# Performance work log

Measured on AMD Instinct MI355X. Metric: run time of the kernel, lower is better.

Reference implementation:

```python
import jax, jax.numpy as jnp
import numpy as np

B, D, H = 131072, 8, 128


def setup_inputs() -> dict:
    key = jax.random.key(0)
    ks = jax.random.split(key, 8)
    s1 = 1.0 / np.sqrt(D + 1)
    s2 = 1.0 / np.sqrt(H)
    return {
        "z": jax.random.normal(ks[0], (B, D), dtype=jnp.float32),
        "logp_z": jnp.zeros((B, 1), dtype=jnp.float32),
        "t": jax.random.uniform(ks[1], (1,), dtype=jnp.float32),
        "W1": jax.random.normal(ks[2], (D + 1, H), dtype=jnp.float32) * s1,
        "b1": jnp.zeros((H,), dtype=jnp.float32),
        "W2": jax.random.normal(ks[3], (H, H), dtype=jnp.float32) * s2,
        "b2": jnp.zeros((H,), dtype=jnp.float32),
        "W3": jax.random.normal(ks[4], (H, D), dtype=jnp.float32) * s2,
        "b3": jnp.zeros((D,), dtype=jnp.float32),
    }


def _net_single(z_i, t_scalar, W1, b1, W2, b2, W3, b3):
    # z_i: [D] -> dz/dt: [D]; FFJORD-style MLP on concat([z, t])
    x = jnp.concatenate([z_i, t_scalar[None]])  # [D+1]
    h = jnp.tanh(x @ W1 + b1)
    h = jnp.tanh(h @ W2 + b2)
    return h @ W3 + b3


def reference(z, logp_z, t, W1, b1, W2, b2, W3, b3):
    t_scalar = t.reshape(())

    def f_i(z_i):
        return _net_single(z_i, t_scalar, W1, b1, W2, b2, W3, b3)

    # dz/dt for every sample (batched forward)
    dz_dt = jax.vmap(f_i)(z)  # [B, D]
    # Exact Jacobian trace: fused forward-mode batched Jacobian (replaces the
    # original's D sequential autograd.grad reverse-mode calls)
    jac = jax.vmap(jax.jacfwd(f_i))(z)  # [B, D, D]
    trace = jnp.einsum("bii->b", jac)  # [B]
    dlogp_z_dt = -trace[:, None]  # [B, 1]
    return (dz_dt, dlogp_z_dt)
```

## Files before the change

### kernel.cpp

```cpp
#include <hip/hip_runtime.h>
#include <hip/hip_bf16.h>

#define BATCH 131072
#define PITCH 136

typedef __bf16 bf16x8 __attribute__((ext_vector_type(8)));
typedef float floatx4 __attribute__((ext_vector_type(4)));

__device__ __forceinline__ float fast_tanh(float x) {
    float e = __expf(2.0f * x);
    return 1.0f - 2.0f * __builtin_amdgcn_rcpf(e + 1.0f);
}


__global__ void prep_kernel(const float* __restrict__ W1,
                            const float* __restrict__ W2,
                            const float* __restrict__ W3,
                            __bf16* __restrict__ ws) {
    int idx = blockIdx.x * 256 + threadIdx.x;
    if (idx < 16384) {
        int j = idx & 7, q = (idx >> 3) & 3, n = (idx >> 5) & 127, kb = idx >> 12;
        int k = kb * 32 + q * 8 + j;
        ws[idx] = (__bf16)W2[k * 128 + n];
        float c = 0.0f;
        #pragma unroll
        for (int d = 0; d < 8; ++d) c += W3[k * 8 + d] * W1[d * 128 + n];
        ws[16384 + idx] = (__bf16)(W2[n * 128 + k] * c);
    } else if (idx < 20480) {
        int t = idx - 16384;
        int j = t & 7, q = (t >> 3) & 3, n = t >> 5;
        int k = q * 8 + j;
        ws[32768 + t] = (k < 9) ? (__bf16)W1[k * 128 + n] : (__bf16)0.0f;
    } else if (idx < 22528) {
        int t = idx - 20480;
        int j = t & 7, q = (t >> 3) & 3, n = (t >> 5) & 15, kb = t >> 9;
        int k = kb * 32 + q * 8 + j;
        ws[36864 + t] = (n < 8) ? (__bf16)W3[k * 8 + n] : (__bf16)0.0f;
    }
}

__global__ __launch_bounds__(256, 2) void cnf_main(
        const float* __restrict__ z, const float* __restrict__ t_ptr,
        const float* __restrict__ b1g, const float* __restrict__ b2g,
        const float* __restrict__ b3g, const __bf16* __restrict__ ws,
        float* __restrict__ out) {
    __shared__ __bf16 sW2s[16384];
    __shared__ __bf16 sW1s[4096];
    __shared__ float sb1[128];
    __shared__ float sb2[128];
    __shared__ __bf16 tile[4][16 * PITCH];

    const int tid = threadIdx.x;
    {
        uint4* dst = (uint4*)sW2s;
        const uint4* src = (const uint4*)ws;
        for (int i = tid; i < 2048; i += 256) dst[i] = src[i];
        uint4* dst1 = (uint4*)sW1s;
        const uint4* src1 = (const uint4*)(ws + 32768);
        for (int i = tid; i < 512; i += 256) dst1[i] = src1[i];
        if (tid < 128) { sb1[tid] = b1g[tid]; sb2[tid] = b2g[tid]; }
    }
    __syncthreads();

    const int lane = tid & 63;
    const int w = tid >> 6;
    const int p = lane & 15;
    const int q = lane >> 4;
    __bf16* T = tile[w];
    const float tval = t_ptr[0];
    const float b3v = (p < 8) ? b3g[p] : 0.0f;
    const bf16x8* W2sv = (const bf16x8*)sW2s;
    const bf16x8* W1sv = (const bf16x8*)sW1s;
    const bf16x8* GTv  = (const bf16x8*)(ws + 16384);
    const bf16x8* W3v  = (const bf16x8*)(ws + 36864);

    for (int it = 0; it < 4; ++it) {
        const int s0 = blockIdx.x * 256 + it * 64 + w * 16;

        bf16x8 ax;
        #pragma unroll
        for (int j = 0; j < 8; ++j) ax[j] = (__bf16)0.0f;
        if (q == 0) {
            const float4 z0 = ((const float4*)(z + (size_t)(s0 + p) * 8))[0];
            const float4 z1 = ((const float4*)(z + (size_t)(s0 + p) * 8))[1];
            ax[0] = (__bf16)z0.x; ax[1] = (__bf16)z0.y;
            ax[2] = (__bf16)z0.z; ax[3] = (__bf16)z0.w;
            ax[4] = (__bf16)z1.x; ax[5] = (__bf16)z1.y;
            ax[6] = (__bf16)z1.z; ax[7] = (__bf16)z1.w;
        } else if (q == 1) {
            ax[0] = (__bf16)tval;
        }

        float a1c[32];
        #pragma unroll
        for (int nt = 0; nt < 8; ++nt) {
            const int n = nt * 16 + p;
            floatx4 acc = {0.f, 0.f, 0.f, 0.f};
            acc = __builtin_amdgcn_mfma_f32_16x16x32_bf16(ax, W1sv[n * 4 + q], acc, 0, 0, 0);
            const float bn = sb1[n];
            #pragma unroll
            for (int r = 0; r < 4; ++r) {
                const float h1 = fast_tanh(acc[r] + bn);
                a1c[nt * 4 + r] = __builtin_fmaf(-h1, h1, 1.0f);
                T[(q * 4 + r) * PITCH + n] = (__bf16)h1;
            }
        }
        bf16x8 ah[4];
        #pragma unroll
        for (int kb = 0; kb < 4; ++kb)
            ah[kb] = *(const bf16x8*)&T[p * PITCH + kb * 32 + q * 8];

        float h2c[32];
        #pragma unroll
        for (int nt = 0; nt < 8; ++nt) {
            const int n = nt * 16 + p;
            floatx4 acc = {0.f, 0.f, 0.f, 0.f};
            #pragma unroll
            for (int kb = 0; kb < 4; ++kb)
                acc = __builtin_amdgcn_mfma_f32_16x16x32_bf16(
                        ah[kb], W2sv[(kb * 128 + n) * 4 + q], acc, 0, 0, 0);
            const float bn = sb2[n];
            #pragma unroll
            for (int r = 0; r < 4; ++r) {
                const float h2 = fast_tanh(acc[r] + bn);
                h2c[nt * 4 + r] = h2;
                const float a2 = __builtin_fmaf(-h2, h2, 1.0f);
                T[(q * 4 + r) * PITCH + n] = (__bf16)a2;
            }
        }
        bf16x8 aa[4];
        #pragma unroll
        for (int kb = 0; kb < 4; ++kb)
            aa[kb] = *(const bf16x8*)&T[p * PITCH + kb * 32 + q * 8];

        float tr[4] = {0.f, 0.f, 0.f, 0.f};
        #pragma unroll
        for (int nt = 0; nt < 8; ++nt) {
            const int n = nt * 16 + p;
            floatx4 acc = {0.f, 0.f, 0.f, 0.f};
            #pragma unroll
            for (int kb = 0; kb < 4; ++kb)
                acc = __builtin_amdgcn_mfma_f32_16x16x32_bf16(
                        aa[kb], GTv[(kb * 128 + n) * 4 + q], acc, 0, 0, 0);
            #pragma unroll
            for (int r = 0; r < 4; ++r)
                tr[r] = __builtin_fmaf(a1c[nt * 4 + r], acc[r], tr[r]);
        }

        #pragma unroll
        for (int i = 0; i < 32; ++i)
            T[(q * 4 + (i & 3)) * PITCH + (i >> 2) * 16 + p] = (__bf16)h2c[i];
        bf16x8 ah2[4];
        #pragma unroll
        for (int kb = 0; kb < 4; ++kb)
            ah2[kb] = *(const bf16x8*)&T[p * PITCH + kb * 32 + q * 8];

        floatx4 acc3 = {0.f, 0.f, 0.f, 0.f};
        #pragma unroll
        for (int kb = 0; kb < 4; ++kb)
            acc3 = __builtin_amdgcn_mfma_f32_16x16x32_bf16(
                    ah2[kb], W3v[(kb * 16 + p) * 4 + q], acc3, 0, 0, 0);
        if (p < 8) {
            #pragma unroll
            for (int r = 0; r < 4; ++r)
                out[(size_t)(s0 + q * 4 + r) * 8 + p] = acc3[r] + b3v;
        }

        #pragma unroll
        for (int r = 0; r < 4; ++r) {
            float v = tr[r];
            v += __shfl_xor(v, 1, 64);
            v += __shfl_xor(v, 2, 64);
            v += __shfl_xor(v, 4, 64);
            v += __shfl_xor(v, 8, 64);
            tr[r] = v;
        }
        if (p == 0) {
            #pragma unroll
            for (int r = 0; r < 4; ++r)
                out[(size_t)BATCH * 8 + s0 + q * 4 + r] = -tr[r];
        }
    }
}

extern "C" void kernel_launch(void* const* d_in, const int* in_sizes, int n_in,
                              void* d_out, int out_size, void* d_ws, size_t ws_size,
                              hipStream_t stream) {
    const float* z  = (const float*)d_in[0];
    const float* t  = (const float*)d_in[2];
    const float* W1 = (const float*)d_in[3];
    const float* b1 = (const float*)d_in[4];
    const float* W2 = (const float*)d_in[5];
    const float* b2 = (const float*)d_in[6];
    const float* W3 = (const float*)d_in[7];
    const float* b3 = (const float*)d_in[8];
    __bf16* ws = (__bf16*)d_ws;
    float* out = (float*)d_out;

    prep_kernel<<<88, 256, 0, stream>>>(W1, W2, W3, ws);
    cnf_main<<<512, 256, 0, stream>>>(z, t, b1, b2, b3, ws, out);
}
```

Before: 104.8 us.

## Read weights from global memory instead of LDS and raise occupancy

Stops staging W2 and W1 in shared memory and has the MFMA operands read them straight from global memory, relying on L1/L2 caching. This shrinks LDS per block so four blocks per CU fit, and the launch bounds and grid double to match (1024 blocks, two iterations each). The layer-2 activations are kept packed as bf16 pairs to cut register pressure. The risk is more global/L2 traffic and latency on the weight loads in exchange for higher occupancy and no per-block staging cost.

```diff
diff --git a/kernel.cpp b/kernel.cpp
--- a/kernel.cpp
+++ b/kernel.cpp
@@ -10,6 +10,12 @@
 __device__ __forceinline__ float fast_tanh(float x) {
     float e = __expf(2.0f * x);
     return 1.0f - 2.0f * __builtin_amdgcn_rcpf(e + 1.0f);
+}
+
+__device__ __forceinline__ unsigned bpack(float a, float b) {
+    unsigned short ua = __builtin_bit_cast(unsigned short, (__bf16)a);
+    unsigned short ub = __builtin_bit_cast(unsigned short, (__bf16)b);
+    return (unsigned)ua | ((unsigned)ub << 16);
 }
 
 
@@ -39,27 +45,17 @@
     }
 }
 
-__global__ __launch_bounds__(256, 2) void cnf_main(
+__global__ __launch_bounds__(256, 4) void cnf_main(
         const float* __restrict__ z, const float* __restrict__ t_ptr,
         const float* __restrict__ b1g, const float* __restrict__ b2g,
         const float* __restrict__ b3g, const __bf16* __restrict__ ws,
         float* __restrict__ out) {
-    __shared__ __bf16 sW2s[16384];
-    __shared__ __bf16 sW1s[4096];
     __shared__ float sb1[128];
     __shared__ float sb2[128];
     __shared__ __bf16 tile[4][16 * PITCH];
 
     const int tid = threadIdx.x;
-    {
-        uint4* dst = (uint4*)sW2s;
-        const uint4* src = (const uint4*)ws;
-        for (int i = tid; i < 2048; i += 256) dst[i] = src[i];
-        uint4* dst1 = (uint4*)sW1s;
-        const uint4* src1 = (const uint4*)(ws + 32768);
-        for (int i = tid; i < 512; i += 256) dst1[i] = src1[i];
-        if (tid < 128) { sb1[tid] = b1g[tid]; sb2[tid] = b2g[tid]; }
-    }
+    if (tid < 128) { sb1[tid] = b1g[tid]; sb2[tid] = b2g[tid]; }
     __syncthreads();
 
     const int lane = tid & 63;
@@ -69,13 +65,14 @@
     __bf16* T = tile[w];
     const float tval = t_ptr[0];
     const float b3v = (p < 8) ? b3g[p] : 0.0f;
-    const bf16x8* W2sv = (const bf16x8*)sW2s;
-    const bf16x8* W1sv = (const bf16x8*)sW1s;
-    const bf16x8* GTv  = (const bf16x8*)(ws + 16384);
-    const bf16x8* W3v  = (const bf16x8*)(ws + 36864);
-
-    for (int it = 0; it < 4; ++it) {
-        const int s0 = blockIdx.x * 256 + it * 64 + w * 16;
+    const bf16x8* W2g = (const bf16x8*)ws;
+    const bf16x8* GTv = (const bf16x8*)(ws + 16384);
+    const bf16x8* W1g = (const bf16x8*)(ws + 32768);
+    const bf16x8* W3v = (const bf16x8*)(ws + 36864);
+
+    #pragma unroll
+    for (int it = 0; it < 2; ++it) {
+        const int s0 = blockIdx.x * 128 + it * 64 + w * 16;
 
         bf16x8 ax;
         #pragma unroll
@@ -96,7 +93,7 @@
         for (int nt = 0; nt < 8; ++nt) {
             const int n = nt * 16 + p;
             floatx4 acc = {0.f, 0.f, 0.f, 0.f};
-            acc = __builtin_amdgcn_mfma_f32_16x16x32_bf16(ax, W1sv[n * 4 + q], acc, 0, 0, 0);
+            acc = __builtin_amdgcn_mfma_f32_16x16x32_bf16(ax, W1g[n * 4 + q], acc, 0, 0, 0);
             const float bn = sb1[n];
             #pragma unroll
             for (int r = 0; r < 4; ++r) {
@@ -110,7 +107,7 @@
         for (int kb = 0; kb < 4; ++kb)
             ah[kb] = *(const bf16x8*)&T[p * PITCH + kb * 32 + q * 8];
 
-        float h2c[32];
+        unsigned h2p[16];
         #pragma unroll
         for (int nt = 0; nt < 8; ++nt) {
             const int n = nt * 16 + p;
@@ -118,15 +115,18 @@
             #pragma unroll
             for (int kb = 0; kb < 4; ++kb)
                 acc = __builtin_amdgcn_mfma_f32_16x16x32_bf16(
-                        ah[kb], W2sv[(kb * 128 + n) * 4 + q], acc, 0, 0, 0);
+                        ah[kb], W2g[(kb * 128 + n) * 4 + q], acc, 0, 0, 0);
             const float bn = sb2[n];
+            float h2v[4];
             #pragma unroll
             for (int r = 0; r < 4; ++r) {
                 const float h2 = fast_tanh(acc[r] + bn);
-                h2c[nt * 4 + r] = h2;
+                h2v[r] = h2;
                 const float a2 = __builtin_fmaf(-h2, h2, 1.0f);
                 T[(q * 4 + r) * PITCH + n] = (__bf16)a2;
             }
+            h2p[nt * 2 + 0] = bpack(h2v[0], h2v[1]);
+            h2p[nt * 2 + 1] = bpack(h2v[2], h2v[3]);
         }
         bf16x8 aa[4];
         #pragma unroll
@@ -148,8 +148,12 @@
         }
 
         #pragma unroll
-        for (int i = 0; i < 32; ++i)
-            T[(q * 4 + (i & 3)) * PITCH + (i >> 2) * 16 + p] = (__bf16)h2c[i];
+        for (int i = 0; i < 16; ++i) {
+            const int nt = i >> 1, rr = (i & 1) * 2;
+            const int base = (q * 4 + rr) * PITCH + nt * 16 + p;
+            T[base]         = __builtin_bit_cast(__bf16, (unsigned short)(h2p[i] & 0xffffu));
+            T[base + PITCH] = __builtin_bit_cast(__bf16, (unsigned short)(h2p[i] >> 16));
+        }
         bf16x8 ah2[4];
         #pragma unroll
         for (int kb = 0; kb < 4; ++kb)
@@ -198,5 +202,5 @@
     float* out = (float*)d_out;
 
     prep_kernel<<<88, 256, 0, stream>>>(W1, W2, W3, ws);
-    cnf_main<<<512, 256, 0, stream>>>(z, t, b1, b2, b3, ws, out);
-}
+    cnf_main<<<1024, 256, 0, stream>>>(z, t, b1, b2, b3, ws, out);
+}
```

After: 151.9 us. 45.0% more time.

## Keep W1 in registers, derive tanh-derivative from h2 tile, double grid size

Applied to the files above, without the earlier changes.

Moves the W1 fragments out of shared memory and into per-lane registers loaded once per block. It also drops the separate h2c register array and second tile write: h2 is stored to the tile once, and both the h2 operand and the (1-h2^2) operand are built from that single read. The grid doubles to 1024 blocks with 2 iterations each for more parallelism, and the tile loops are fully unrolled. The aim is fewer LDS writes, lower register pressure, and better occupancy and latency hiding, at the cost of reloading W2 into LDS in twice as many blocks. The derivative is now computed from the bf16-rounded h2, which slightly changes rounding.

```diff
diff --git a/kernel.cpp b/kernel.cpp
--- a/kernel.cpp
+++ b/kernel.cpp
@@ -45,7 +45,6 @@
         const float* __restrict__ b3g, const __bf16* __restrict__ ws,
         float* __restrict__ out) {
     __shared__ __bf16 sW2s[16384];
-    __shared__ __bf16 sW1s[4096];
     __shared__ float sb1[128];
     __shared__ float sb2[128];
     __shared__ __bf16 tile[4][16 * PITCH];
@@ -54,10 +53,8 @@
     {
         uint4* dst = (uint4*)sW2s;
         const uint4* src = (const uint4*)ws;
-        for (int i = tid; i < 2048; i += 256) dst[i] = src[i];
-        uint4* dst1 = (uint4*)sW1s;
-        const uint4* src1 = (const uint4*)(ws + 32768);
-        for (int i = tid; i < 512; i += 256) dst1[i] = src1[i];
+        #pragma unroll
+        for (int i = 0; i < 8; ++i) dst[tid + i * 256] = src[tid + i * 256];
         if (tid < 128) { sb1[tid] = b1g[tid]; sb2[tid] = b2g[tid]; }
     }
     __syncthreads();
@@ -70,12 +67,17 @@
     const float tval = t_ptr[0];
     const float b3v = (p < 8) ? b3g[p] : 0.0f;
     const bf16x8* W2sv = (const bf16x8*)sW2s;
-    const bf16x8* W1sv = (const bf16x8*)sW1s;
     const bf16x8* GTv  = (const bf16x8*)(ws + 16384);
+    const bf16x8* W1g  = (const bf16x8*)(ws + 32768);
     const bf16x8* W3v  = (const bf16x8*)(ws + 36864);
 
-    for (int it = 0; it < 4; ++it) {
-        const int s0 = blockIdx.x * 256 + it * 64 + w * 16;
+    bf16x8 w1f[8];
+    #pragma unroll
+    for (int nt = 0; nt < 8; ++nt) w1f[nt] = W1g[(nt * 16 + p) * 4 + q];
+
+    #pragma unroll
+    for (int it = 0; it < 2; ++it) {
+        const int s0 = blockIdx.x * 128 + it * 64 + w * 16;
 
         bf16x8 ax;
         #pragma unroll
@@ -96,7 +98,7 @@
         for (int nt = 0; nt < 8; ++nt) {
             const int n = nt * 16 + p;
             floatx4 acc = {0.f, 0.f, 0.f, 0.f};
-            acc = __builtin_amdgcn_mfma_f32_16x16x32_bf16(ax, W1sv[n * 4 + q], acc, 0, 0, 0);
+            acc = __builtin_amdgcn_mfma_f32_16x16x32_bf16(ax, w1f[nt], acc, 0, 0, 0);
             const float bn = sb1[n];
             #pragma unroll
             for (int r = 0; r < 4; ++r) {
@@ -110,7 +112,6 @@
         for (int kb = 0; kb < 4; ++kb)
             ah[kb] = *(const bf16x8*)&T[p * PITCH + kb * 32 + q * 8];
 
-        float h2c[32];
         #pragma unroll
         for (int nt = 0; nt < 8; ++nt) {
             const int n = nt * 16 + p;
@@ -123,37 +124,20 @@
             #pragma unroll
             for (int r = 0; r < 4; ++r) {
                 const float h2 = fast_tanh(acc[r] + bn);
-                h2c[nt * 4 + r] = h2;
-                const float a2 = __builtin_fmaf(-h2, h2, 1.0f);
-                T[(q * 4 + r) * PITCH + n] = (__bf16)a2;
+                T[(q * 4 + r) * PITCH + n] = (__bf16)h2;
             }
         }
+        bf16x8 ah2[4];
         bf16x8 aa[4];
         #pragma unroll
-        for (int kb = 0; kb < 4; ++kb)
-            aa[kb] = *(const bf16x8*)&T[p * PITCH + kb * 32 + q * 8];
-
-        float tr[4] = {0.f, 0.f, 0.f, 0.f};
-        #pragma unroll
-        for (int nt = 0; nt < 8; ++nt) {
-            const int n = nt * 16 + p;
-            floatx4 acc = {0.f, 0.f, 0.f, 0.f};
-            #pragma unroll
-            for (int kb = 0; kb < 4; ++kb)
-                acc = __builtin_amdgcn_mfma_f32_16x16x32_bf16(
-                        aa[kb], GTv[(kb * 128 + n) * 4 + q], acc, 0, 0, 0);
-            #pragma unroll
-            for (int r = 0; r < 4; ++r)
-                tr[r] = __builtin_fmaf(a1c[nt * 4 + r], acc[r], tr[r]);
-        }
-
-        #pragma unroll
-        for (int i = 0; i < 32; ++i)
-            T[(q * 4 + (i & 3)) * PITCH + (i >> 2) * 16 + p] = (__bf16)h2c[i];
-        bf16x8 ah2[4];
-        #pragma unroll
-        for (int kb = 0; kb < 4; ++kb)
+        for (int kb = 0; kb < 4; ++kb) {
             ah2[kb] = *(const bf16x8*)&T[p * PITCH + kb * 32 + q * 8];
+            #pragma unroll
+            for (int j = 0; j < 8; ++j) {
+                const float f = (float)ah2[kb][j];
+                aa[kb][j] = (__bf16)__builtin_fmaf(-f, f, 1.0f);
+            }
+        }
 
         floatx4 acc3 = {0.f, 0.f, 0.f, 0.f};
         #pragma unroll
@@ -164,6 +148,20 @@
             #pragma unroll
             for (int r = 0; r < 4; ++r)
                 out[(size_t)(s0 + q * 4 + r) * 8 + p] = acc3[r] + b3v;
+        }
+
+        float tr[4] = {0.f, 0.f, 0.f, 0.f};
+        #pragma unroll
+        for (int nt = 0; nt < 8; ++nt) {
+            const int n = nt * 16 + p;
+            floatx4 acc = {0.f, 0.f, 0.f, 0.f};
+            #pragma unroll
+            for (int kb = 0; kb < 4; ++kb)
+                acc = __builtin_amdgcn_mfma_f32_16x16x32_bf16(
+                        aa[kb], GTv[(kb * 128 + n) * 4 + q], acc, 0, 0, 0);
+            #pragma unroll
+            for (int r = 0; r < 4; ++r)
+                tr[r] = __builtin_fmaf(a1c[nt * 4 + r], acc[r], tr[r]);
         }
 
         #pragma unroll
@@ -198,5 +196,5 @@
     float* out = (float*)d_out;
 
     prep_kernel<<<88, 256, 0, stream>>>(W1, W2, W3, ws);
-    cnf_main<<<512, 256, 0, stream>>>(z, t, b1, b2, b3, ws, out);
-}
+    cnf_main<<<1024, 256, 0, stream>>>(z, t, b1, b2, b3, ws, out);
+}
```

Result: no change. 105.6 us (+0.8%).
